# Kernel optimization log

Measured on AMD Instinct MI355X. Metric: run time of the kernel, lower is better.

The kernel has to match this reference:

```python
import jax, jax.numpy as jnp
import numpy as np

HEAD_COUNT = 16
HEAD_DIM = 128  # embed_count // head_count = 2048 // 16


def setup_inputs() -> dict:
    key = jax.random.key(0)
    k0, k1, k2, k3, k4 = jax.random.split(key, 5)
    B, C, S = 4, 2048, 1024
    keys = jax.random.normal(k0, (B, C, 1, S), dtype=jnp.float32)
    values = jax.random.normal(k1, (B, C, 1, S), dtype=jnp.float32)
    queries = jax.random.normal(k2, (B, C, 1, S), dtype=jnp.float32)
    attention_mask = jax.random.randint(k3, (B, S), 0, 2).astype(bool)
    # guarantee at least one valid key per batch row so softmax is finite
    attention_mask = attention_mask.at[:, 0].set(True)
    w_out = jax.random.normal(k4, (C, C), dtype=jnp.float32) * 0.02
    return {"keys": keys, "values": values, "queries": queries,
            "attention_mask": attention_mask, "w_out": w_out}


def reference(keys, values, queries, attention_mask, w_out):
    B, C, _, S = keys.shape
    h, d = HEAD_COUNT, HEAD_DIM
    # keys: [B,C,1,S] -> transpose(1,3) -> [B,S,1,C] -> [B,S,h,d]
    k = jnp.transpose(keys[:, :, 0, :], (0, 2, 1)).reshape(B, S, h, d)      # bkhd
    # values/queries: [B,C,1,S] -> [B,h,d,S] -> transpose(1,2) -> [B,d,h,S]
    v = jnp.transpose(values[:, :, 0, :].reshape(B, h, d, S), (0, 2, 1, 3))  # bdhk
    q = jnp.transpose(queries[:, :, 0, :].reshape(B, h, d, S), (0, 2, 1, 3)) # bdhq
    # additive mask bias: 0 where attended, -inf where masked; broadcast over h,q
    bias = jnp.where(attention_mask, 0.0, -jnp.inf).astype(keys.dtype)       # [B,K]
    scale = 1.0 / np.sqrt(d).astype(np.float32)
    w = jnp.einsum('bdhq,bkhd->bkhq', q * scale, k)                          # [B,K,h,Q]
    w = w + bias[:, :, None, None]
    w = jax.nn.softmax(w, axis=1)  # softmax over keys (dim 1)
    hid = jnp.einsum('bkhq,bdhk->bdhq', w, v)                                # [B,d,h,Q]
    hid = jnp.transpose(hid, (0, 2, 1, 3)).reshape(B, C, S)                  # [B,C,Q]
    out = jnp.einsum('oc,bcq->boq', w_out, hid)                              # 1x1 conv out_proj
    return out.reshape(B, C, 1, S)
```

## Files before the change

### kernel.cpp

```cpp
#include <hip/hip_runtime.h>

#define Bq 4
#define Cc 2048
#define Ss 1024
#define Hh 16
#define Dd 128

#define QSCALE 0.127517429f

typedef __bf16 bf16x8 __attribute__((ext_vector_type(8)));
typedef float  f32x4  __attribute__((ext_vector_type(4)));

__device__ __forceinline__ ushort f2bf(float f) {
    uint u = __float_as_uint(f);
    u += 0x7FFFu + ((u >> 16) & 1u);
    return (ushort)(u >> 16);
}
__device__ __forceinline__ uint pack2bf(float a, float b) {
    return (uint)f2bf(a) | ((uint)f2bf(b) << 16);
}
__device__ __forceinline__ void gld16(const void* g, void* l) {
    __builtin_amdgcn_global_load_lds(
        (const __attribute__((address_space(1))) unsigned int*)g,
        (__attribute__((address_space(3))) unsigned int*)l, 16, 0, 0);
}

__global__ __launch_bounds__(256) void mask_bias_k(const unsigned* __restrict__ mask,
                                                   float* __restrict__ bias) {
    __shared__ int f01, ff;
    const int t = threadIdx.x;
    if (t == 0) { f01 = 0; ff = 0; }
    __syncthreads();
    int a = 0, b = 0;
    for (int i = t; i < 1024; i += 256) {
        unsigned v = mask[i];
        if (v != 0u && v != 1u) a = 1;
        if (v != 0u && v != 0x3F800000u) b = 1;
    }
    if (a) atomicOr(&f01, 1);
    if (b) atomicOr(&ff, 1);
    __syncthreads();
    const int mode = f01 ? (ff ? 1 : 2) : 0;
    const int* mi = (const int*)mask;
    const unsigned char* mb = (const unsigned char*)mask;
    const float* mf = (const float*)mask;
    for (int i = t; i < Bq * Ss; i += 256) {
        bool on;
        if (mode == 0)      on = (mi[i] != 0);
        else if (mode == 1) on = (mb[i] != 0);
        else                on = (mf[i] != 0.0f);
        bias[i] = on ? 0.0f : -1e30f;
    }
}

__global__ __launch_bounds__(256) void wcvt_swz(const float* __restrict__ w,
                                                ushort* __restrict__ wb) {
    const size_t e = ((size_t)blockIdx.x * 256 + threadIdx.x) * 8;
    const int row = (int)(e >> 11), col = (int)(e & 2047);
    const int colS = (col & ~63) | ((col & 63) ^ ((row & 7) << 3));
    float4 v0 = *(const float4*)&w[e];
    float4 v1 = *(const float4*)&w[e + 4];
    uint4 o;
    o.x = pack2bf(v0.x, v0.y); o.y = pack2bf(v0.z, v0.w);
    o.z = pack2bf(v1.x, v1.y); o.w = pack2bf(v1.z, v1.w);
    *(uint4*)&wb[(size_t)row * 2048 + colS] = o;
}

__global__ __launch_bounds__(256) void vcvt_perm(const float* __restrict__ v,
                                                 ushort* __restrict__ vb) {
    const int tid = blockIdx.x * 256 + threadIdx.x;
    const int row = tid >> 7;
    const int cp = tid & 127;
    const int blk = (cp >> 3) * 64;
    const int j0 = cp & 7;
    const int b5 = j0 >> 2, h = j0 & 3;
    const float* src = v + (size_t)row * 1024 + blk + 32 * b5 + 4 * h;
    float4 A = *(const float4*)src;
    float4 B = *(const float4*)(src + 16);
    uint4 o;
    o.x = pack2bf(A.x, A.y); o.y = pack2bf(A.z, A.w);
    o.z = pack2bf(B.x, B.y); o.w = pack2bf(B.z, B.w);
    *(uint4*)&vb[(size_t)row * 1024 + blk + ((j0 * 8) ^ ((row & 7) << 3))] = o;
}

__global__ __launch_bounds__(256) void qk_prep(const float* __restrict__ queries,
                                               const float* __restrict__ keys,
                                               ushort* __restrict__ Qt,
                                               ushort* __restrict__ Kt) {
    __shared__ float T[128][65];
    const int t = threadIdx.x;
    const int s0 = blockIdx.x * 64;
    const int bh = blockIdx.y;
    const int isK = blockIdx.z;
    const float* src = (isK ? keys : queries) + (size_t)bh * 128 * 1024;
    const float sc = isK ? 1.0f : QSCALE;

#pragma unroll
    for (int p = 0; p < 8; ++p) {
        const int d = p * 16 + (t >> 4);
        float4 v = *(const float4*)&src[(size_t)d * 1024 + s0 + (t & 15) * 4];
        T[d][(t & 15) * 4 + 0] = v.x * sc;
        T[d][(t & 15) * 4 + 1] = v.y * sc;
        T[d][(t & 15) * 4 + 2] = v.z * sc;
        T[d][(t & 15) * 4 + 3] = v.w * sc;
    }
    __syncthreads();

    ushort* outp = isK ? Kt : Qt;
#pragma unroll
    for (int p = 0; p < 4; ++p) {
        const int k = p * 16 + (t >> 4);
        const int x = t & 15;
        uint4 o;
        o.x = pack2bf(T[x * 8 + 0][k], T[x * 8 + 1][k]);
        o.y = pack2bf(T[x * 8 + 2][k], T[x * 8 + 3][k]);
        o.z = pack2bf(T[x * 8 + 4][k], T[x * 8 + 5][k]);
        o.w = pack2bf(T[x * 8 + 6][k], T[x * 8 + 7][k]);
        const size_t rowbyte = ((size_t)bh * 1024 + s0 + k) * 256;
        const int boff = isK ? ((x * 16) ^ ((k & 7) << 4)) : (x * 16);
        *(uint4*)((char*)outp + rowbyte + boff) = o;
    }
}

__global__ __launch_bounds__(256) void attn4(const ushort* __restrict__ Qt,
                                             const ushort* __restrict__ Kt,
                                             const ushort* __restrict__ Vbf,
                                             const float* __restrict__ bias,
                                             ushort* __restrict__ hidT) {
    __shared__ __align__(16) char SMEM[69632];
    ushort* KT2  = (ushort*)SMEM;
    ushort* Vs2  = (ushort*)(SMEM + 32768);
    float*  biasS = (float*)(SMEM + 65536);

    const int t = threadIdx.x, l = t & 63, w = t >> 6;
    const int kk = l & 15, g = l >> 4;

    const int bid = blockIdx.x;
    const int vid = (bid & 7) * 64 + (bid >> 3);
    const int bh = vid >> 3, qt = vid & 7;
    const int b = bh >> 4;
    const int q0 = qt * 128;
    const size_t bhbase = (size_t)bh * 1024;

    for (int i = t; i < Ss; i += 256) biasS[i] = bias[b * Ss + i];

    bf16x8 qf[2][4];
#pragma unroll
    for (int qs = 0; qs < 2; ++qs) {
        const ushort* qrow = Qt + (bhbase + q0 + w * 32 + qs * 16 + kk) * 128;
#pragma unroll
        for (int dc = 0; dc < 4; ++dc)
            qf[qs][dc] = *(const bf16x8*)(qrow + dc * 32 + g * 8);
    }

    float lrun[2] = {0.0f, 0.0f};
    f32x4 hacc[2][8];
#pragma unroll
    for (int qs = 0; qs < 2; ++qs)
#pragma unroll
        for (int i = 0; i < 8; ++i) hacc[qs][i] = (f32x4){0.f, 0.f, 0.f, 0.f};

#define ATTN_STAGE(bufi, cki)                                                   \
    {                                                                           \
        const int k0n = (cki) * 64;                                             \
        _Pragma("unroll")                                                       \
        for (int ii = 0; ii < 4; ++ii) {                                        \
            const int ik = ii * 4 + w;                                          \
            gld16(Kt + (bhbase + k0n + ik * 4 + (l >> 4)) * 128 + (l & 15) * 8, \
                  KT2 + (bufi) * 8192 + ik * 512);                              \
            gld16(Vbf + ((size_t)bh * 128 + ik * 8 + (l >> 3)) * 1024 + k0n +   \
                      (l & 7) * 8,                                              \
                  Vs2 + (bufi) * 8192 + ik * 512);                              \
        }                                                                       \
    }

    ATTN_STAGE(0, 0);
    __syncthreads();

    int buf = 0;
    for (int ck = 0; ck < 16; ++ck) {
        const int k0 = ck * 64;
        if (ck + 1 < 16) ATTN_STAGE(buf ^ 1, ck + 1);

        const ushort* KTb = KT2 + buf * 8192;
        const ushort* Vsb = Vs2 + buf * 8192;

        f32x4 sc[2][4];
        __builtin_amdgcn_s_setprio(1);
#pragma unroll
        for (int ns = 0; ns < 4; ++ns) {
            bf16x8 kf[4];
            const ushort* kr = KTb + (ns * 16 + kk) * 128;
#pragma unroll
            for (int dc = 0; dc < 4; ++dc)
                kf[dc] = *(const bf16x8*)(kr + ((dc * 32 + g * 8) ^ ((kk & 7) << 3)));
#pragma unroll
            for (int qs = 0; qs < 2; ++qs) {
                f32x4 a = (f32x4){0.f, 0.f, 0.f, 0.f};
#pragma unroll
                for (int dc = 0; dc < 4; ++dc)
                    a = __builtin_amdgcn_mfma_f32_16x16x32_bf16(kf[dc], qf[qs][dc], a, 0, 0, 0);
                sc[qs][ns] = a;
            }
        }
        __builtin_amdgcn_s_setprio(0);

        float4 bk4[4];
#pragma unroll
        for (int ns = 0; ns < 4; ++ns)
            bk4[ns] = *(const float4*)&biasS[k0 + ns * 16 + g * 4];

        bf16x8 pb[2][2];
#pragma unroll
        for (int qs = 0; qs < 2; ++qs) {
            float pv[4][4];
            float s = 0.0f;
#pragma unroll
            for (int ns = 0; ns < 4; ++ns) {
                const float* bb = (const float*)&bk4[ns];
#pragma unroll
                for (int r = 0; r < 4; ++r) {
                    float p = exp2f(sc[qs][ns][r] + bb[r]);
                    pv[ns][r] = p;
                    s += p;
                }
            }
            lrun[qs] += s;
#pragma unroll
            for (int kh = 0; kh < 2; ++kh) {
                bf16x8 vpk;
#pragma unroll
                for (int j = 0; j < 8; ++j)
                    vpk[j] = (__bf16)pv[2 * kh + (j >> 2)][j & 3];
                pb[qs][kh] = vpk;
            }
        }

        __builtin_amdgcn_s_setprio(1);
#pragma unroll
        for (int kh = 0; kh < 2; ++kh) {
#pragma unroll
            for (int ds = 0; ds < 8; ++ds) {
                bf16x8 vf = *(const bf16x8*)(Vsb + (ds * 16 + kk) * 64 +
                                             ((kh * 32 + g * 8) ^ ((kk & 7) << 3)));
                hacc[0][ds] = __builtin_amdgcn_mfma_f32_16x16x32_bf16(vf, pb[0][kh], hacc[0][ds], 0, 0, 0);
                hacc[1][ds] = __builtin_amdgcn_mfma_f32_16x16x32_bf16(vf, pb[1][kh], hacc[1][ds], 0, 0, 0);
            }
        }
        __builtin_amdgcn_s_setprio(0);

        asm volatile("s_waitcnt vmcnt(0)" ::: "memory");
        __builtin_amdgcn_s_barrier();
        buf ^= 1;
    }
#undef ATTN_STAGE

    float linv[2];
#pragma unroll
    for (int qs = 0; qs < 2; ++qs) {
        float s = lrun[qs];
        s += __shfl_xor(s, 16);
        s += __shfl_xor(s, 32);
        linv[qs] = 1.0f / s;
    }

    {
        ushort* hs = (ushort*)SMEM;
#pragma unroll
        for (int qs = 0; qs < 2; ++qs) {
            const int row = w * 32 + qs * 16 + kk;
#pragma unroll
            for (int ds = 0; ds < 8; ++ds) {
                uint2 pk;
                pk.x = pack2bf(hacc[qs][ds][0] * linv[qs], hacc[qs][ds][1] * linv[qs]);
                pk.y = pack2bf(hacc[qs][ds][2] * linv[qs], hacc[qs][ds][3] * linv[qs]);
                const int off = row * 256 + ((ds * 32 + g * 8) ^ ((row & 7) << 4));
                *(uint2*)((char*)hs + off) = pk;
            }
        }
    }
    __syncthreads();

    const int hh = bh & 15;
    const char* hsb = (const char*)SMEM;
#pragma unroll
    for (int it = 0; it < 8; ++it) {
        const int idx = it * 256 + t;
        const int q = idx >> 4, x = idx & 15;
        uint4 vv = *(const uint4*)(hsb + q * 256 + x * 16);
        *(uint4*)((char*)hidT + ((size_t)(b * Ss + q0 + q)) * 4096 + hh * 256 + x * 16) = vv;
    }
}

__global__ __launch_bounds__(512, 4) void proj2(const ushort* __restrict__ Wbf,
                                                const ushort* __restrict__ hidT,
                                                float* __restrict__ out) {
    __shared__ __align__(16) ushort Wl[2][128 * 64];
    __shared__ __align__(16) ushort Hl[2][128 * 64];
    const int t = threadIdx.x, l = t & 63, w = t >> 6;
    const int kk = l & 15, g = l >> 4;
    const int wr = w >> 2, wc = w & 3;

    const int bid = blockIdx.x;
    const int vid = (bid & 7) * 64 + (bid >> 3);
    const int o0 = (vid & 15) * 128;
    const int n0 = (vid >> 4) * 128;

    f32x4 acc[4][2];
#pragma unroll
    for (int i = 0; i < 4; ++i)
#pragma unroll
        for (int j = 0; j < 2; ++j) acc[i][j] = (f32x4){0.f, 0.f, 0.f, 0.f};

#define PROJ_STAGE(buf, ks)                                                        \
    {                                                                              \
        _Pragma("unroll")                                                          \
        for (int ii = 0; ii < 4; ++ii) {                                           \
            const int inst = ii * 8 + w;                                           \
            if (inst < 16) {                                                       \
                const int r = inst * 8 + (l >> 3);                                 \
                gld16(Wbf + ((size_t)(o0 + r) * Cc + (ks) * 64) + (l & 7) * 8,     \
                      &Wl[buf][inst * 512]);                                       \
            } else {                                                               \
                const int i2 = inst - 16;                                          \
                const int r = i2 * 8 + (l >> 3);                                   \
                gld16(hidT + ((size_t)(n0 + r) * Cc + (ks) * 64) + (l & 7) * 8,    \
                      &Hl[buf][i2 * 512]);                                         \
            }                                                                      \
        }                                                                          \
    }

    PROJ_STAGE(0, 0);
    asm volatile("s_waitcnt vmcnt(0)" ::: "memory");
    __builtin_amdgcn_s_barrier();

    int cur = 0;
    for (int ks = 0; ks < 32; ++ks) {
        if (ks + 1 < 32) PROJ_STAGE(cur ^ 1, ks + 1);
        bf16x8 af[2][4], bf[2][2];
#pragma unroll
        for (int dc = 0; dc < 2; ++dc) {
#pragma unroll
            for (int ms = 0; ms < 4; ++ms) {
                const int row = wr * 64 + ms * 16 + kk;
                af[dc][ms] = *(const bf16x8*)&Wl[cur][row * 64 +
                                 ((dc * 32 + g * 8) ^ ((kk & 7) << 3))];
            }
#pragma unroll
            for (int ns = 0; ns < 2; ++ns) {
                const int row = wc * 32 + ns * 16 + kk;
                bf[dc][ns] = *(const bf16x8*)&Hl[cur][row * 64 +
                                 ((dc * 32 + g * 8) ^ ((kk & 7) << 3))];
            }
        }
        __builtin_amdgcn_s_setprio(1);
#pragma unroll
        for (int dc = 0; dc < 2; ++dc)
#pragma unroll
            for (int ms = 0; ms < 4; ++ms)
#pragma unroll
                for (int ns = 0; ns < 2; ++ns)
                    acc[ms][ns] = __builtin_amdgcn_mfma_f32_16x16x32_bf16(
                        af[dc][ms], bf[dc][ns], acc[ms][ns], 0, 0, 0);
        __builtin_amdgcn_s_setprio(0);
        asm volatile("s_waitcnt vmcnt(0) lgkmcnt(0)" ::: "memory");
        __builtin_amdgcn_s_barrier();
        cur ^= 1;
    }
#undef PROJ_STAGE

#pragma unroll
    for (int ms = 0; ms < 4; ++ms)
#pragma unroll
        for (int ns = 0; ns < 2; ++ns) {
            const int o = o0 + wr * 64 + ms * 16 + g * 4;
            const int n = n0 + wc * 32 + ns * 16 + kk;
            const int bb = n >> 10, qq = n & 1023;
            float* op = out + ((size_t)(bb * Cc + o)) * Ss + qq;
#pragma unroll
            for (int r = 0; r < 4; ++r) op[(size_t)r * Ss] = acc[ms][ns][r];
        }
}

extern "C" void kernel_launch(void* const* d_in, const int* in_sizes, int n_in,
                              void* d_out, int out_size, void* d_ws, size_t ws_size,
                              hipStream_t stream) {
    const float*    keys    = (const float*)d_in[0];
    const float*    values  = (const float*)d_in[1];
    const float*    queries = (const float*)d_in[2];
    const unsigned* mask    = (const unsigned*)d_in[3];
    const float*    w_out   = (const float*)d_in[4];
    float* out = (float*)d_out;

    char* ws = (char*)d_ws;
    float*  bias = (float*)ws;
    ushort* Wbf  = (ushort*)(ws + 16384);
    ushort* Qt   = (ushort*)(ws + 16384 + (8u << 20));
    ushort* Kt   = (ushort*)(ws + 16384 + (24u << 20));
    ushort* Vbf  = (ushort*)(ws + 16384 + (40u << 20));
    ushort* hidT = (ushort*)(ws + 16384 + (56u << 20));

    hipLaunchKernelGGL(mask_bias_k, dim3(1), dim3(256), 0, stream, mask, bias);
    hipLaunchKernelGGL(wcvt_swz, dim3(2048), dim3(256), 0, stream, w_out, Wbf);
    hipLaunchKernelGGL(vcvt_perm, dim3(4096), dim3(256), 0, stream, values, Vbf);
    hipLaunchKernelGGL(qk_prep, dim3(16, 64, 2), dim3(256), 0, stream,
                       queries, keys, Qt, Kt);
    hipLaunchKernelGGL(attn4, dim3(512), dim3(256), 0, stream,
                       Qt, Kt, Vbf, bias, hidT);
    hipLaunchKernelGGL(proj2, dim3(512), dim3(512), 0, stream,
                       Wbf, hidT, out);
}
```

Baseline: 129.4 us.

## Enlarge attention and projection tiles and switch to triple-buffered async loads

The attention kernel now uses 512-thread blocks covering 256 queries, so each K/V chunk staged in LDS serves twice as many queries. Loads run in a three-stage ring with partial vmcnt waits, so two chunks are in flight while one is computed. The projection kernel moves to 256x128 output tiles with a 4x4 MFMA accumulator per wave and the same triple-buffered pipeline. The grids shrink to 256 blocks each, which may underfill a 256-CU part, and LDS use grows to about 100 KB and 144 KB per block, which limits occupancy.

```diff
diff --git a/kernel.cpp b/kernel.cpp
--- a/kernel.cpp
+++ b/kernel.cpp
@@ -122,27 +122,25 @@
     }
 }
 
-__global__ __launch_bounds__(256) void attn4(const ushort* __restrict__ Qt,
-                                             const ushort* __restrict__ Kt,
-                                             const ushort* __restrict__ Vbf,
-                                             const float* __restrict__ bias,
-                                             ushort* __restrict__ hidT) {
-    __shared__ __align__(16) char SMEM[69632];
-    ushort* KT2  = (ushort*)SMEM;
-    ushort* Vs2  = (ushort*)(SMEM + 32768);
-    float*  biasS = (float*)(SMEM + 65536);
+__global__ __launch_bounds__(512, 2) void attn5(const ushort* __restrict__ Qt,
+                                                const ushort* __restrict__ Kt,
+                                                const ushort* __restrict__ Vbf,
+                                                const float* __restrict__ bias,
+                                                ushort* __restrict__ hidT) {
+    __shared__ __align__(16) char SMEM[102400];
+    float* biasS = (float*)(SMEM + 98304);
 
     const int t = threadIdx.x, l = t & 63, w = t >> 6;
     const int kk = l & 15, g = l >> 4;
 
     const int bid = blockIdx.x;
-    const int vid = (bid & 7) * 64 + (bid >> 3);
-    const int bh = vid >> 3, qt = vid & 7;
+    const int vid = (bid & 7) * 32 + (bid >> 3);
+    const int bh = vid >> 2, qt = vid & 3;
     const int b = bh >> 4;
-    const int q0 = qt * 128;
+    const int q0 = qt * 256;
     const size_t bhbase = (size_t)bh * 1024;
 
-    for (int i = t; i < Ss; i += 256) biasS[i] = bias[b * Ss + i];
+    for (int i = t; i < Ss; i += 512) biasS[i] = bias[b * Ss + i];
 
     bf16x8 qf[2][4];
 #pragma unroll
@@ -163,97 +161,116 @@
 #define ATTN_STAGE(bufi, cki)                                                   \
     {                                                                           \
         const int k0n = (cki) * 64;                                             \
+        ushort* Kd = (ushort*)SMEM + (bufi) * 8192;                             \
+        ushort* Vd = (ushort*)(SMEM + 49152) + (bufi) * 8192;                   \
         _Pragma("unroll")                                                       \
         for (int ii = 0; ii < 4; ++ii) {                                        \
-            const int ik = ii * 4 + w;                                          \
-            gld16(Kt + (bhbase + k0n + ik * 4 + (l >> 4)) * 128 + (l & 15) * 8, \
-                  KT2 + (bufi) * 8192 + ik * 512);                              \
-            gld16(Vbf + ((size_t)bh * 128 + ik * 8 + (l >> 3)) * 1024 + k0n +   \
-                      (l & 7) * 8,                                              \
-                  Vs2 + (bufi) * 8192 + ik * 512);                              \
+            const int inst = ii * 8 + w;                                        \
+            if (inst < 16) {                                                    \
+                gld16(Kt + (bhbase + k0n + inst * 4 + (l >> 4)) * 128 +         \
+                          (l & 15) * 8,                                         \
+                      Kd + inst * 512);                                         \
+            } else {                                                            \
+                const int i2 = inst - 16;                                       \
+                gld16(Vbf + ((size_t)bh * 128 + i2 * 8 + (l >> 3)) * 1024 +     \
+                          k0n + (l & 7) * 8,                                    \
+                      Vd + i2 * 512);                                           \
+            }                                                                   \
         }                                                                       \
     }
 
+#define ATTN_COMPUTE(bi, ck)                                                     \
+    {                                                                            \
+        const int k0 = (ck) * 64;                                                \
+        const ushort* KTb = (const ushort*)SMEM + (bi) * 8192;                   \
+        const ushort* Vsb = (const ushort*)(SMEM + 49152) + (bi) * 8192;         \
+        f32x4 sc[2][4];                                                          \
+        __builtin_amdgcn_s_setprio(1);                                           \
+        _Pragma("unroll")                                                        \
+        for (int ns = 0; ns < 4; ++ns) {                                         \
+            bf16x8 kf[4];                                                        \
+            const ushort* kr = KTb + (ns * 16 + kk) * 128;                       \
+            _Pragma("unroll")                                                    \
+            for (int dc = 0; dc < 4; ++dc)                                       \
+                kf[dc] = *(const bf16x8*)(kr +                                   \
+                             ((dc * 32 + g * 8) ^ ((kk & 7) << 3)));             \
+            _Pragma("unroll")                                                    \
+            for (int qs = 0; qs < 2; ++qs) {                                     \
+                f32x4 a = (f32x4){0.f, 0.f, 0.f, 0.f};                           \
+                _Pragma("unroll")                                                \
+                for (int dc = 0; dc < 4; ++dc)                                   \
+                    a = __builtin_amdgcn_mfma_f32_16x16x32_bf16(                 \
+                        kf[dc], qf[qs][dc], a, 0, 0, 0);                         \
+                sc[qs][ns] = a;                                                  \
+            }                                                                    \
+        }                                                                        \
+        __builtin_amdgcn_s_setprio(0);                                           \
+        float4 bk4[4];                                                           \
+        _Pragma("unroll")                                                        \
+        for (int ns = 0; ns < 4; ++ns)                                           \
+            bk4[ns] = *(const float4*)&biasS[k0 + ns * 16 + g * 4];              \
+        bf16x8 pb[2][2];                                                         \
+        _Pragma("unroll")                                                        \
+        for (int qs = 0; qs < 2; ++qs) {                                         \
+            float pv[4][4];                                                      \
+            float s = 0.0f;                                                      \
+            _Pragma("unroll")                                                    \
+            for (int ns = 0; ns < 4; ++ns) {                                     \
+                const float* bb2 = (const float*)&bk4[ns];                       \
+                _Pragma("unroll")                                                \
+                for (int r = 0; r < 4; ++r) {                                    \
+                    float p = exp2f(sc[qs][ns][r] + bb2[r]);                     \
+                    pv[ns][r] = p;                                               \
+                    s += p;                                                      \
+                }                                                                \
+            }                                                                    \
+            lrun[qs] += s;                                                       \
+            _Pragma("unroll")                                                    \
+            for (int kh = 0; kh < 2; ++kh) {                                     \
+                bf16x8 vpk;                                                      \
+                _Pragma("unroll")                                                \
+                for (int j = 0; j < 8; ++j)                                      \
+                    vpk[j] = (__bf16)pv[2 * kh + (j >> 2)][j & 3];               \
+                pb[qs][kh] = vpk;                                                \
+            }                                                                    \
+        }                                                                        \
+        __builtin_amdgcn_s_setprio(1);                                           \
+        _Pragma("unroll")                                                        \
+        for (int kh = 0; kh < 2; ++kh) {                                         \
+            _Pragma("unroll")                                                    \
+            for (int ds = 0; ds < 8; ++ds) {                                     \
+                bf16x8 vf = *(const bf16x8*)(Vsb + (ds * 16 + kk) * 64 +         \
+                                 ((kh * 32 + g * 8) ^ ((kk & 7) << 3)));         \
+                hacc[0][ds] = __builtin_amdgcn_mfma_f32_16x16x32_bf16(           \
+                    vf, pb[0][kh], hacc[0][ds], 0, 0, 0);                        \
+                hacc[1][ds] = __builtin_amdgcn_mfma_f32_16x16x32_bf16(           \
+                    vf, pb[1][kh], hacc[1][ds], 0, 0, 0);                        \
+            }                                                                    \
+        }                                                                        \
+        __builtin_amdgcn_s_setprio(0);                                           \
+    }
+
     ATTN_STAGE(0, 0);
-    __syncthreads();
-
-    int buf = 0;
-    for (int ck = 0; ck < 16; ++ck) {
-        const int k0 = ck * 64;
-        if (ck + 1 < 16) ATTN_STAGE(buf ^ 1, ck + 1);
-
-        const ushort* KTb = KT2 + buf * 8192;
-        const ushort* Vsb = Vs2 + buf * 8192;
-
-        f32x4 sc[2][4];
-        __builtin_amdgcn_s_setprio(1);
-#pragma unroll
-        for (int ns = 0; ns < 4; ++ns) {
-            bf16x8 kf[4];
-            const ushort* kr = KTb + (ns * 16 + kk) * 128;
-#pragma unroll
-            for (int dc = 0; dc < 4; ++dc)
-                kf[dc] = *(const bf16x8*)(kr + ((dc * 32 + g * 8) ^ ((kk & 7) << 3)));
-#pragma unroll
-            for (int qs = 0; qs < 2; ++qs) {
-                f32x4 a = (f32x4){0.f, 0.f, 0.f, 0.f};
-#pragma unroll
-                for (int dc = 0; dc < 4; ++dc)
-                    a = __builtin_amdgcn_mfma_f32_16x16x32_bf16(kf[dc], qf[qs][dc], a, 0, 0, 0);
-                sc[qs][ns] = a;
-            }
-        }
-        __builtin_amdgcn_s_setprio(0);
-
-        float4 bk4[4];
-#pragma unroll
-        for (int ns = 0; ns < 4; ++ns)
-            bk4[ns] = *(const float4*)&biasS[k0 + ns * 16 + g * 4];
-
-        bf16x8 pb[2][2];
-#pragma unroll
-        for (int qs = 0; qs < 2; ++qs) {
-            float pv[4][4];
-            float s = 0.0f;
-#pragma unroll
-            for (int ns = 0; ns < 4; ++ns) {
-                const float* bb = (const float*)&bk4[ns];
-#pragma unroll
-                for (int r = 0; r < 4; ++r) {
-                    float p = exp2f(sc[qs][ns][r] + bb[r]);
-                    pv[ns][r] = p;
-                    s += p;
-                }
-            }
-            lrun[qs] += s;
-#pragma unroll
-            for (int kh = 0; kh < 2; ++kh) {
-                bf16x8 vpk;
-#pragma unroll
-                for (int j = 0; j < 8; ++j)
-                    vpk[j] = (__bf16)pv[2 * kh + (j >> 2)][j & 3];
-                pb[qs][kh] = vpk;
-            }
-        }
-
-        __builtin_amdgcn_s_setprio(1);
-#pragma unroll
-        for (int kh = 0; kh < 2; ++kh) {
-#pragma unroll
-            for (int ds = 0; ds < 8; ++ds) {
-                bf16x8 vf = *(const bf16x8*)(Vsb + (ds * 16 + kk) * 64 +
-                                             ((kh * 32 + g * 8) ^ ((kk & 7) << 3)));
-                hacc[0][ds] = __builtin_amdgcn_mfma_f32_16x16x32_bf16(vf, pb[0][kh], hacc[0][ds], 0, 0, 0);
-                hacc[1][ds] = __builtin_amdgcn_mfma_f32_16x16x32_bf16(vf, pb[1][kh], hacc[1][ds], 0, 0, 0);
-            }
-        }
-        __builtin_amdgcn_s_setprio(0);
-
-        asm volatile("s_waitcnt vmcnt(0)" ::: "memory");
+    ATTN_STAGE(1, 1);
+    asm volatile("s_waitcnt vmcnt(4)" ::: "memory");
+    __builtin_amdgcn_s_barrier();
+
+    int cb = 0, sb = 2;
+    for (int ck = 0; ck < 14; ++ck) {
+        ATTN_STAGE(sb, ck + 2);
+        ATTN_COMPUTE(cb, ck);
+        asm volatile("s_waitcnt vmcnt(4)" ::: "memory");
         __builtin_amdgcn_s_barrier();
-        buf ^= 1;
-    }
+        cb = (cb == 2) ? 0 : cb + 1;
+        sb = (sb == 2) ? 0 : sb + 1;
+    }
+    ATTN_COMPUTE(cb, 14);
+    asm volatile("s_waitcnt vmcnt(0)" ::: "memory");
+    __builtin_amdgcn_s_barrier();
+    cb = (cb == 2) ? 0 : cb + 1;
+    ATTN_COMPUTE(cb, 15);
 #undef ATTN_STAGE
+#undef ATTN_COMPUTE
 
     float linv[2];
 #pragma unroll
@@ -264,6 +281,7 @@
         linv[qs] = 1.0f / s;
     }
 
+    __syncthreads();
     {
         ushort* hs = (ushort*)SMEM;
 #pragma unroll
@@ -285,96 +303,110 @@
     const char* hsb = (const char*)SMEM;
 #pragma unroll
     for (int it = 0; it < 8; ++it) {
-        const int idx = it * 256 + t;
+        const int idx = it * 512 + t;
         const int q = idx >> 4, x = idx & 15;
         uint4 vv = *(const uint4*)(hsb + q * 256 + x * 16);
         *(uint4*)((char*)hidT + ((size_t)(b * Ss + q0 + q)) * 4096 + hh * 256 + x * 16) = vv;
     }
 }
 
-__global__ __launch_bounds__(512, 4) void proj2(const ushort* __restrict__ Wbf,
+__global__ __launch_bounds__(512, 2) void proj3(const ushort* __restrict__ Wbf,
                                                 const ushort* __restrict__ hidT,
                                                 float* __restrict__ out) {
-    __shared__ __align__(16) ushort Wl[2][128 * 64];
-    __shared__ __align__(16) ushort Hl[2][128 * 64];
+    __shared__ __align__(16) char SMEM[147456];
     const int t = threadIdx.x, l = t & 63, w = t >> 6;
     const int kk = l & 15, g = l >> 4;
-    const int wr = w >> 2, wc = w & 3;
+    const int wr = w >> 1, wc = w & 1;
 
     const int bid = blockIdx.x;
-    const int vid = (bid & 7) * 64 + (bid >> 3);
-    const int o0 = (vid & 15) * 128;
-    const int n0 = (vid >> 4) * 128;
-
-    f32x4 acc[4][2];
+    const int vid = (bid & 7) * 32 + (bid >> 3);
+    const int o0 = (vid >> 5) * 256;
+    const int n0 = (vid & 31) * 128;
+
+    f32x4 acc[4][4];
 #pragma unroll
     for (int i = 0; i < 4; ++i)
 #pragma unroll
-        for (int j = 0; j < 2; ++j) acc[i][j] = (f32x4){0.f, 0.f, 0.f, 0.f};
-
-#define PROJ_STAGE(buf, ks)                                                        \
+        for (int j = 0; j < 4; ++j) acc[i][j] = (f32x4){0.f, 0.f, 0.f, 0.f};
+
+#define PROJ_STAGE(bufi, ks)                                                       \
     {                                                                              \
+        ushort* Wd = (ushort*)SMEM + (bufi) * 16384;                               \
+        ushort* Hd = (ushort*)(SMEM + 98304) + (bufi) * 8192;                      \
         _Pragma("unroll")                                                          \
-        for (int ii = 0; ii < 4; ++ii) {                                           \
+        for (int ii = 0; ii < 6; ++ii) {                                           \
             const int inst = ii * 8 + w;                                           \
-            if (inst < 16) {                                                       \
-                const int r = inst * 8 + (l >> 3);                                 \
-                gld16(Wbf + ((size_t)(o0 + r) * Cc + (ks) * 64) + (l & 7) * 8,     \
-                      &Wl[buf][inst * 512]);                                       \
+            if (inst < 32) {                                                       \
+                gld16(Wbf + ((size_t)(o0 + inst * 8 + (l >> 3)) * 2048) +          \
+                          (ks) * 64 + (l & 7) * 8,                                 \
+                      Wd + inst * 512);                                            \
             } else {                                                               \
-                const int i2 = inst - 16;                                          \
-                const int r = i2 * 8 + (l >> 3);                                   \
-                gld16(hidT + ((size_t)(n0 + r) * Cc + (ks) * 64) + (l & 7) * 8,    \
-                      &Hl[buf][i2 * 512]);                                         \
+                const int j = inst - 32;                                           \
+                gld16(hidT + ((size_t)(n0 + j * 8 + (l >> 3)) * 2048) +            \
+                          (ks) * 64 + (l & 7) * 8,                                 \
+                      Hd + j * 512);                                               \
             }                                                                      \
         }                                                                          \
     }
 
+#define PROJ_COMPUTE(bi)                                                           \
+    {                                                                              \
+        const ushort* Wb2 = (const ushort*)SMEM + (bi) * 16384;                    \
+        const ushort* Hb2 = (const ushort*)(SMEM + 98304) + (bi) * 8192;           \
+        _Pragma("unroll")                                                          \
+        for (int dc = 0; dc < 2; ++dc) {                                           \
+            bf16x8 af[4], bf[4];                                                   \
+            _Pragma("unroll")                                                      \
+            for (int ms = 0; ms < 4; ++ms) {                                       \
+                const int row = wr * 64 + ms * 16 + kk;                            \
+                af[ms] = *(const bf16x8*)&Wb2[row * 64 +                           \
+                             ((dc * 32 + g * 8) ^ ((kk & 7) << 3))];               \
+            }                                                                      \
+            _Pragma("unroll")                                                      \
+            for (int ns = 0; ns < 4; ++ns) {                                       \
+                const int row = wc * 64 + ns * 16 + kk;                            \
+                bf[ns] = *(const bf16x8*)&Hb2[row * 64 +                           \
+                             ((dc * 32 + g * 8) ^ ((kk & 7) << 3))];               \
+            }                                                                      \
+            __builtin_amdgcn_s_setprio(1);                                         \
+            _Pragma("unroll")                                                      \
+            for (int ms = 0; ms < 4; ++ms)                                         \
+                _Pragma("unroll")                                                  \
+                for (int ns = 0; ns < 4; ++ns)                                     \
+                    acc[ms][ns] = __builtin_amdgcn_mfma_f32_16x16x32_bf16(         \
+                        af[ms], bf[ns], acc[ms][ns], 0, 0, 0);                     \
+            __builtin_amdgcn_s_setprio(0);                                         \
+        }                                                                          \
+    }
+
     PROJ_STAGE(0, 0);
+    PROJ_STAGE(1, 1);
+    asm volatile("s_waitcnt vmcnt(6)" ::: "memory");
+    __builtin_amdgcn_s_barrier();
+
+    int cb = 0, sbuf = 2;
+    for (int ks = 0; ks < 30; ++ks) {
+        PROJ_STAGE(sbuf, ks + 2);
+        PROJ_COMPUTE(cb);
+        asm volatile("s_waitcnt vmcnt(6)" ::: "memory");
+        __builtin_amdgcn_s_barrier();
+        cb = (cb == 2) ? 0 : cb + 1;
+        sbuf = (sbuf == 2) ? 0 : sbuf + 1;
+    }
+    PROJ_COMPUTE(cb);
     asm volatile("s_waitcnt vmcnt(0)" ::: "memory");
     __builtin_amdgcn_s_barrier();
-
-    int cur = 0;
-    for (int ks = 0; ks < 32; ++ks) {
-        if (ks + 1 < 32) PROJ_STAGE(cur ^ 1, ks + 1);
-        bf16x8 af[2][4], bf[2][2];
-#pragma unroll
-        for (int dc = 0; dc < 2; ++dc) {
-#pragma unroll
-            for (int ms = 0; ms < 4; ++ms) {
-                const int row = wr * 64 + ms * 16 + kk;
-                af[dc][ms] = *(const bf16x8*)&Wl[cur][row * 64 +
-                                 ((dc * 32 + g * 8) ^ ((kk & 7) << 3))];
-            }
-#pragma unroll
-            for (int ns = 0; ns < 2; ++ns) {
-                const int row = wc * 32 + ns * 16 + kk;
-                bf[dc][ns] = *(const bf16x8*)&Hl[cur][row * 64 +
-                                 ((dc * 32 + g * 8) ^ ((kk & 7) << 3))];
-            }
-        }
-        __builtin_amdgcn_s_setprio(1);
-#pragma unroll
-        for (int dc = 0; dc < 2; ++dc)
-#pragma unroll
-            for (int ms = 0; ms < 4; ++ms)
-#pragma unroll
-                for (int ns = 0; ns < 2; ++ns)
-                    acc[ms][ns] = __builtin_amdgcn_mfma_f32_16x16x32_bf16(
-                        af[dc][ms], bf[dc][ns], acc[ms][ns], 0, 0, 0);
-        __builtin_amdgcn_s_setprio(0);
-        asm volatile("s_waitcnt vmcnt(0) lgkmcnt(0)" ::: "memory");
-        __builtin_amdgcn_s_barrier();
-        cur ^= 1;
-    }
+    cb = (cb == 2) ? 0 : cb + 1;
+    PROJ_COMPUTE(cb);
 #undef PROJ_STAGE
+#undef PROJ_COMPUTE
 
 #pragma unroll
     for (int ms = 0; ms < 4; ++ms)
 #pragma unroll
-        for (int ns = 0; ns < 2; ++ns) {
+        for (int ns = 0; ns < 4; ++ns) {
             const int o = o0 + wr * 64 + ms * 16 + g * 4;
-            const int n = n0 + wc * 32 + ns * 16 + kk;
+            const int n = n0 + wc * 64 + ns * 16 + kk;
             const int bb = n >> 10, qq = n & 1023;
             float* op = out + ((size_t)(bb * Cc + o)) * Ss + qq;
 #pragma unroll
@@ -405,8 +437,8 @@
     hipLaunchKernelGGL(vcvt_perm, dim3(4096), dim3(256), 0, stream, values, Vbf);
     hipLaunchKernelGGL(qk_prep, dim3(16, 64, 2), dim3(256), 0, stream,
                        queries, keys, Qt, Kt);
-    hipLaunchKernelGGL(attn4, dim3(512), dim3(256), 0, stream,
+    hipLaunchKernelGGL(attn5, dim3(256), dim3(512), 0, stream,
                        Qt, Kt, Vbf, bias, hidT);
-    hipLaunchKernelGGL(proj2, dim3(512), dim3(512), 0, stream,
+    hipLaunchKernelGGL(proj3, dim3(256), dim3(512), 0, stream,
                        Wbf, hidT, out);
 }
```

Result: faster. 125.7 us (-2.9%).
